# Kernel optimization log

Hardware: AMD Instinct MI355X
Metric: run time of the kernel (lower is better)

The kernel has to match this reference:

```python
import jax, jax.numpy as jnp
import numpy as np

B, T, N_EMBD = 1, 2048, 2048
N_HEAD = 16
KV_LOW = 512      # kv_low_rank == head_size (compressed value dim)
Q_LOW = 1024
ROPE_HS = 64
QK_HS = KV_LOW + ROPE_HS  # 576
HEAD_SIZE = KV_LOW        # v_equiv = c_kv.view(B,1,T,head_size)


def _rope_tables(seq_len, dim, base=10000.0):
    # litgpt-style: theta over half dim, duplicated to full dim
    inv = 1.0 / (base ** (np.arange(0, dim, 2, dtype=np.float32) / dim))
    t = np.arange(seq_len, dtype=np.float32)
    freqs = np.outer(t, inv)                      # [T, dim/2]
    emb = np.concatenate([freqs, freqs], axis=-1)  # [T, dim]
    return jnp.asarray(np.cos(emb)), jnp.asarray(np.sin(emb))


def _apply_rope(x, cos, sin):
    # x: [..., T, d]; cos/sin broadcastable [T, d]. rotate-half RoPE.
    d = x.shape[-1]
    x1, x2 = x[..., : d // 2], x[..., d // 2:]
    rotated = jnp.concatenate([-x2, x1], axis=-1)
    return x * cos + rotated * sin


def setup_inputs() -> dict:
    key = jax.random.key(0)
    ks = jax.random.split(key, 4)
    x = jax.random.normal(ks[0], (B, T, N_EMBD), dtype=jnp.float32)
    cos, sin = _rope_tables(T, ROPE_HS)
    s = 0.02
    W_qkv = jax.random.normal(ks[1], (N_EMBD, KV_LOW + ROPE_HS + Q_LOW), dtype=jnp.float32) * s
    W_qdec = jax.random.normal(ks[2], (Q_LOW, N_HEAD * QK_HS), dtype=jnp.float32) * s
    W_out = jax.random.normal(ks[3], (N_HEAD * HEAD_SIZE, N_EMBD), dtype=jnp.float32) * s
    return {"x": x, "cos": cos, "sin": sin, "W_qkv": W_qkv, "W_qdec": W_qdec, "W_out": W_out}


def reference(x, cos, sin, W_qkv, W_qdec, W_out):
    Bq, Tq, _ = x.shape
    # latent encoding and split
    latents = x @ W_qkv                                       # [B,T,kv+rope+q]
    c_kv = latents[..., :KV_LOW]                              # [B,T,512] (keys-nope and values)
    k_r = latents[..., KV_LOW:KV_LOW + ROPE_HS]               # [B,T,64]
    c_q = latents[..., KV_LOW + ROPE_HS:]                     # [B,T,1024]
    # per-head query decode
    q = (c_q @ W_qdec).reshape(Bq, Tq, N_HEAD, QK_HS)         # [B,T,H,576]
    q_nope, q_r = q[..., :KV_LOW], q[..., KV_LOW:]
    # partial RoPE
    k_r = _apply_rope(k_r, cos, sin)                          # [B,T,64]
    q_r = _apply_rope(q_r, cos[None, :, None, :], sin[None, :, None, :])  # [B,T,H,64]
    q = jnp.concatenate([q_nope, q_r], axis=-1)               # [B,T,H,576]
    q = jnp.swapaxes(q, 1, 2)                                 # [B,H,T,576]
    k = jnp.concatenate([c_kv, k_r], axis=-1)                 # [B,T,576] shared across heads
    v = c_kv                                                  # [B,T,512] shared across heads
    scale = 1.0 / jnp.sqrt(jnp.float32(HEAD_SIZE))
    scores = jnp.einsum('bhtd,bsd->bhts', q, k) * scale       # [B,H,T,T]
    causal = jnp.tril(jnp.ones((Tq, Tq), dtype=bool))
    scores = jnp.where(causal, scores, jnp.finfo(scores.dtype).min)
    attn = jax.nn.softmax(scores, axis=-1)
    y = jnp.einsum('bhts,bsd->bhtd', attn, v)                 # [B,H,T,512]
    y = jnp.swapaxes(y, 1, 2).reshape(Bq, Tq, N_HEAD * HEAD_SIZE)
    return y @ W_out                                          # [B,T,n_embd]
```

## Files before the change

### kernel.cpp

```cpp
#include <hip/hip_runtime.h>

typedef __bf16 bf16x8_t __attribute__((ext_vector_type(8)));
typedef float f32x4_t __attribute__((ext_vector_type(4)));

#define LAT_LD 1664
#define QK_DIM 576
#define V_DIM 512
#define NHEAD 16
#define TSEQ 2048
#define QLD 9216
#define YLD 8192
#define SCALE 0.044194173824159216f

__device__ __forceinline__ unsigned short f2bf(float f) {
  union { float f; unsigned int u; } v; v.f = f;
  unsigned int r = v.u + 0x7FFFu + ((v.u >> 16) & 1u);
  return (unsigned short)(r >> 16);
}

__device__ __forceinline__ void load_lds16(const unsigned short* g, unsigned short* l) {
  __builtin_amdgcn_global_load_lds((const __attribute__((address_space(1))) void*)g,
                                   (__attribute__((address_space(3))) void*)l, 16, 0, 0);
}

__global__ __launch_bounds__(256) void conv_flat(const float* __restrict__ src,
                                                 unsigned short* __restrict__ dst, int n) {
  int i = (blockIdx.x * 256 + threadIdx.x) * 4;
  if (i < n) {
    float4 v = *(const float4*)&src[i];
    ushort4 o;
    o.x = f2bf(v.x); o.y = f2bf(v.y); o.z = f2bf(v.z); o.w = f2bf(v.w);
    *(ushort4*)&dst[i] = o;
  }
}

__global__ __launch_bounds__(256) void conv_t(const float* __restrict__ src, int R, int Csrc,
                                              unsigned short* __restrict__ dst) {
  __shared__ unsigned short T[64][72];
  const int tid = threadIdx.x;
  const int r0 = blockIdx.x * 64, c0 = blockIdx.y * 64;
  const bool live = (c0 < Csrc);
#pragma unroll
  for (int it = 0; it < 4; ++it) {
    int idx = it * 256 + tid;
    int c4 = (idx >> 6) * 4;
    int r = idx & 63;
    float4 v = {0.f, 0.f, 0.f, 0.f};
    if (live) v = *(const float4*)&src[(size_t)(r0 + r) * Csrc + c0 + c4];
    T[c4 + 0][r] = f2bf(v.x);
    T[c4 + 1][r] = f2bf(v.y);
    T[c4 + 2][r] = f2bf(v.z);
    T[c4 + 3][r] = f2bf(v.w);
  }
  __syncthreads();
#pragma unroll
  for (int it = 0; it < 2; ++it) {
    int idx = it * 256 + tid;
    int cc = idx >> 3, r8 = (idx & 7) * 8;
    uint4 v = *(const uint4*)&T[cc][r8];
    *(uint4*)&dst[(size_t)(c0 + cc) * R + r0 + r8] = v;
  }
}

__global__ __launch_bounds__(256) void vtrans(const unsigned short* __restrict__ lat,
                                              unsigned short* __restrict__ vtg) {
  __shared__ unsigned short T[64][72];
  const int tid = threadIdx.x;
  const int r0 = blockIdx.x * 64, c0 = blockIdx.y * 64;
#pragma unroll
  for (int it = 0; it < 2; ++it) {
    int idx = it * 256 + tid;
    int c8 = (idx >> 6) * 8;
    int r = idx & 63;
    uint4 v = *(const uint4*)&lat[(size_t)(r0 + r) * LAT_LD + c0 + c8];
    unsigned short* pv = (unsigned short*)&v;
#pragma unroll
    for (int j = 0; j < 8; ++j) T[c8 + j][r] = pv[j];
  }
  __syncthreads();
#pragma unroll
  for (int it = 0; it < 2; ++it) {
    int idx = it * 256 + tid;
    int cc = idx >> 3, r8 = (idx & 7) * 8;
    uint4 v = *(const uint4*)&T[cc][r8];
    *(uint4*)&vtg[(size_t)(c0 + cc) * TSEQ + r0 + r8] = v;
  }
}

#define GEMM_PROLOGUE()                                                     \
  __shared__ __align__(16) unsigned short As[4096];                         \
  __shared__ __align__(16) unsigned short Bs[4096];                         \
  const int tid = threadIdx.x;                                              \
  const int wave = tid >> 6, lane = tid & 63;                               \
  const int quad = lane >> 4, l16 = lane & 15;                              \
  const int wm = wave >> 1, wn = wave & 1;                                  \
  f32x4_t acc[4][4];                                                        \
  f32x4_t zero = {0.f, 0.f, 0.f, 0.f};                                      \
  _Pragma("unroll") for (int mi = 0; mi < 4; ++mi)                          \
    _Pragma("unroll") for (int ni = 0; ni < 4; ++ni) acc[mi][ni] = zero;

#define GEMM_KLOOP(Aptr, Alda, Bptr, Bldb, M0, N0, KLEN)                    \
  for (int k0 = 0; k0 < (KLEN); k0 += 32) {                                 \
    _Pragma("unroll") for (int p2 = 0; p2 < 2; ++p2) {                      \
      int ci = p2 * 256 + tid;                                              \
      int rr2 = ci >> 2, cc2 = (ci & 3) * 8;                                \
      load_lds16(&(Aptr)[(size_t)((M0) + rr2) * (Alda) + k0 + cc2], &As[ci * 8]); \
      load_lds16(&(Bptr)[(size_t)((N0) + rr2) * (Bldb) + k0 + cc2], &Bs[ci * 8]); \
    }                                                                       \
    __syncthreads();                                                        \
    bf16x8_t af[4], bfr[4];                                                 \
    _Pragma("unroll") for (int mi = 0; mi < 4; ++mi)                        \
      af[mi] = *(const bf16x8_t*)&As[(wm * 64 + mi * 16 + l16) * 32 + quad * 8]; \
    _Pragma("unroll") for (int ni = 0; ni < 4; ++ni)                        \
      bfr[ni] = *(const bf16x8_t*)&Bs[(wn * 64 + ni * 16 + l16) * 32 + quad * 8]; \
    _Pragma("unroll") for (int mi = 0; mi < 4; ++mi)                        \
      _Pragma("unroll") for (int ni = 0; ni < 4; ++ni)                      \
        acc[mi][ni] = __builtin_amdgcn_mfma_f32_16x16x32_bf16(af[mi], bfr[ni], acc[mi][ni], 0, 0, 0); \
    __syncthreads();                                                        \
  }

template <int OUTF32>
__global__ __launch_bounds__(256, 2) void gemm_bt(
    const unsigned short* __restrict__ A, int lda,
    const unsigned short* __restrict__ Bt, int ldb,
    void* __restrict__ C, int ldc, int K) {
  const int m0 = blockIdx.y * 128, n0 = blockIdx.x * 128;
  GEMM_PROLOGUE();
  GEMM_KLOOP(A, lda, Bt, ldb, m0, n0, K);
#pragma unroll
  for (int mi = 0; mi < 4; ++mi)
#pragma unroll
    for (int ni = 0; ni < 4; ++ni)
#pragma unroll
      for (int r = 0; r < 4; ++r) {
        int row = m0 + wm * 64 + mi * 16 + quad * 4 + r;
        int col = n0 + wn * 64 + ni * 16 + l16;
        if (OUTF32)
          ((float*)C)[(size_t)row * ldc + col] = acc[mi][ni][r];
        else
          ((unsigned short*)C)[(size_t)row * ldc + col] = f2bf(acc[mi][ni][r]);
      }
}

__global__ __launch_bounds__(256, 2) void gemm_splitk(
    const unsigned short* __restrict__ A, int lda,
    const unsigned short* __restrict__ Bt, int ldb,
    float* __restrict__ P, int ldc, int Ks) {
  const int m0 = blockIdx.y * 128, n0 = blockIdx.x * 128;
  const size_t koff = (size_t)blockIdx.z * Ks;
  const unsigned short* Ap = A + koff;
  const unsigned short* Bp = Bt + koff;
  float* C = P + (size_t)blockIdx.z * ((size_t)gridDim.y * 128) * ldc;
  GEMM_PROLOGUE();
  GEMM_KLOOP(Ap, lda, Bp, ldb, m0, n0, Ks);
#pragma unroll
  for (int mi = 0; mi < 4; ++mi)
#pragma unroll
    for (int ni = 0; ni < 4; ++ni)
#pragma unroll
      for (int r = 0; r < 4; ++r) {
        int row = m0 + wm * 64 + mi * 16 + quad * 4 + r;
        int col = n0 + wn * 64 + ni * 16 + l16;
        C[(size_t)row * ldc + col] = acc[mi][ni][r];
      }
}

__global__ __launch_bounds__(256) void reduce2_bf(const float* __restrict__ p,
                                                  unsigned short* __restrict__ dst, int n) {
  int i = (blockIdx.x * 256 + threadIdx.x) * 4;
  if (i < n) {
    float4 a = *(const float4*)&p[i];
    float4 b = *(const float4*)&p[(size_t)n + i];
    ushort4 o;
    o.x = f2bf(a.x + b.x); o.y = f2bf(a.y + b.y);
    o.z = f2bf(a.z + b.z); o.w = f2bf(a.w + b.w);
    *(ushort4*)&dst[i] = o;
  }
}

__global__ __launch_bounds__(256) void reduce4_f32(const float* __restrict__ p,
                                                   float* __restrict__ dst, int n) {
  int i = (blockIdx.x * 256 + threadIdx.x) * 4;
  if (i < n) {
    float4 a = *(const float4*)&p[i];
    float4 b = *(const float4*)&p[(size_t)n + i];
    float4 c = *(const float4*)&p[2 * (size_t)n + i];
    float4 d = *(const float4*)&p[3 * (size_t)n + i];
    float4 o;
    o.x = (a.x + b.x) + (c.x + d.x);
    o.y = (a.y + b.y) + (c.y + d.y);
    o.z = (a.z + b.z) + (c.z + d.z);
    o.w = (a.w + b.w) + (c.w + d.w);
    *(float4*)&dst[i] = o;
  }
}

__global__ __launch_bounds__(256, 2) void qke_kernel(
    const unsigned short* __restrict__ qbuf,
    const unsigned short* __restrict__ lat,
    unsigned short* __restrict__ Ebuf,
    float* __restrict__ lsum, int tq0, int tq1) {
  int tx = blockIdx.x, i_l = 0, cnt = tq0 + 1;
  while (tx >= cnt) { tx -= cnt; ++i_l; ++cnt; }
  const int j = tx;
  const int ig = tq0 + i_l;
  const int h = blockIdx.y;
  const int Kp = tq1 << 7;
  const int Rp = (tq1 - tq0) << 7;
  const int r0g = ig << 7;

  const unsigned short* A = qbuf + (size_t)r0g * QLD + h * QK_DIM;
  const unsigned short* Bt = lat + (size_t)(j << 7) * LAT_LD;
  unsigned short* Eh = Ebuf + (size_t)h * Rp * Kp;

  GEMM_PROLOGUE();
  GEMM_KLOOP(A, QLD, Bt, LAT_LD, 0, 0, QK_DIM);

#pragma unroll
  for (int mi = 0; mi < 4; ++mi) {
    float rs[4] = {0.f, 0.f, 0.f, 0.f};
#pragma unroll
    for (int ni = 0; ni < 4; ++ni)
#pragma unroll
      for (int r = 0; r < 4; ++r) {
        int qr = r0g + wm * 64 + mi * 16 + quad * 4 + r;
        int key = (j << 7) + wn * 64 + ni * 16 + l16;
        float e = (key <= qr) ? __expf(acc[mi][ni][r] * SCALE) : 0.f;
        rs[r] += e;
        Eh[(size_t)(qr - (tq0 << 7)) * Kp + key] = f2bf(e);
      }
#pragma unroll
    for (int r = 0; r < 4; ++r) {
      float s = rs[r];
#pragma unroll
      for (int off = 1; off < 16; off <<= 1) s += __shfl_xor(s, off, 64);
      if (l16 == 0) {
        int qr = r0g + wm * 64 + mi * 16 + quad * 4 + r;
        atomicAdd(&lsum[h * TSEQ + qr], s);
      }
    }
  }
}

__global__ __launch_bounds__(256, 2) void pv_kernel(
    const unsigned short* __restrict__ Ebuf,
    const unsigned short* __restrict__ vtg,
    const float* __restrict__ lsum,
    unsigned short* __restrict__ ybuf, int tq0, int tq1) {
  const int i_l = blockIdx.y, h = blockIdx.z;
  const int n0 = blockIdx.x * 128;
  const int Kp = tq1 << 7;
  const int Rp = (tq1 - tq0) << 7;
  const int Kmax = (tq0 + i_l + 1) << 7;

  const unsigned short* A = Ebuf + (size_t)h * Rp * Kp + (size_t)(i_l << 7) * Kp;
  const unsigned short* Bt = vtg;

  GEMM_PROLOGUE();
  GEMM_KLOOP(A, Kp, Bt, TSEQ, 0, n0, Kmax);

#pragma unroll
  for (int mi = 0; mi < 4; ++mi)
#pragma unroll
    for (int r = 0; r < 4; ++r) {
      int row_g = ((tq0 + i_l) << 7) + wm * 64 + mi * 16 + quad * 4 + r;
      float inv = 1.f / lsum[h * TSEQ + row_g];
#pragma unroll
      for (int ni = 0; ni < 4; ++ni) {
        int col = h * V_DIM + n0 + wn * 64 + ni * 16 + l16;
        ybuf[(size_t)row_g * YLD + col] = f2bf(acc[mi][ni][r] * inv);
      }
    }
}

__global__ __launch_bounds__(256) void rope_k(unsigned short* __restrict__ lat,
                                              const float* __restrict__ cosb,
                                              const float* __restrict__ sinb) {
  int idx = blockIdx.x * 256 + threadIdx.x;
  if (idx >= TSEQ * 32) return;
  int t = idx >> 5, d = idx & 31;
  unsigned short* p = &lat[(size_t)t * LAT_LD + 512];
  union { unsigned int u; float f; } a, b;
  a.u = ((unsigned int)p[d]) << 16; b.u = ((unsigned int)p[d + 32]) << 16;
  float c0 = cosb[t * 64 + d], s0 = sinb[t * 64 + d];
  float c1 = cosb[t * 64 + d + 32], s1 = sinb[t * 64 + d + 32];
  p[d] = f2bf(a.f * c0 - b.f * s0);
  p[d + 32] = f2bf(b.f * c1 + a.f * s1);
}

__global__ __launch_bounds__(256) void rope_q(unsigned short* __restrict__ q,
                                              const float* __restrict__ cosb,
                                              const float* __restrict__ sinb) {
  int idx = blockIdx.x * 256 + threadIdx.x;
  if (idx >= TSEQ * NHEAD * 32) return;
  int t = idx >> 9, h = (idx >> 5) & 15, d = idx & 31;
  unsigned short* p = &q[(size_t)t * QLD + h * QK_DIM + 512];
  union { unsigned int u; float f; } a, b;
  a.u = ((unsigned int)p[d]) << 16; b.u = ((unsigned int)p[d + 32]) << 16;
  float c0 = cosb[t * 64 + d], s0 = sinb[t * 64 + d];
  float c1 = cosb[t * 64 + d + 32], s1 = sinb[t * 64 + d + 32];
  p[d] = f2bf(a.f * c0 - b.f * s0);
  p[d + 32] = f2bf(b.f * c1 + a.f * s1);
}

extern "C" void kernel_launch(void* const* d_in, const int* in_sizes, int n_in,
                              void* d_out, int out_size, void* d_ws, size_t ws_size,
                              hipStream_t stream) {
  (void)in_sizes; (void)n_in; (void)out_size; (void)ws_size;
  const float* x     = (const float*)d_in[0];
  const float* cosb  = (const float*)d_in[1];
  const float* sinb  = (const float*)d_in[2];
  const float* wqkv  = (const float*)d_in[3];
  const float* wqdec = (const float*)d_in[4];
  const float* wout  = (const float*)d_in[5];
  float* out = (float*)d_out;

  unsigned short* ws     = (unsigned short*)d_ws;
  unsigned short* xb     = ws;
  unsigned short* wqkvT  = xb     + (size_t)2048 * 2048;
  unsigned short* wqdecT = wqkvT  + (size_t)1664 * 2048;
  unsigned short* lat    = wqdecT + (size_t)9216 * 1024;
  unsigned short* qbuf   = lat    + (size_t)2048 * 1664;
  unsigned short* woutT  = qbuf   + (size_t)2048 * 9216;
  unsigned short* ybuf   = woutT  + (size_t)2048 * 8192;
  unsigned short* vtg    = ybuf   + (size_t)2048 * 8192;
  float*          lsumf  = (float*)(vtg + (size_t)512 * 2048);
  unsigned short* Ebuf   = ws;
  float*          P1     = (float*)qbuf;
  float*          Pf     = (float*)ws;

  conv_flat<<<4096, 256, 0, stream>>>(x, xb, 2048 * 2048);
  conv_t<<<dim3(32, 26), 256, 0, stream>>>(wqkv, 2048, 1600, wqkvT);
  conv_t<<<dim3(16, 144), 256, 0, stream>>>(wqdec, 1024, 9216, wqdecT);
  conv_t<<<dim3(128, 32), 256, 0, stream>>>(wout, 8192, 2048, woutT);
  hipMemsetAsync(lsumf, 0, NHEAD * TSEQ * sizeof(float), stream);

  gemm_splitk<<<dim3(13, 16, 2), 256, 0, stream>>>(xb, 2048, wqkvT, 2048, P1, 1664, 1024);
  reduce2_bf<<<3328, 256, 0, stream>>>(P1, lat, 2048 * 1664);
  rope_k<<<256, 256, 0, stream>>>(lat, cosb, sinb);
  vtrans<<<dim3(32, 8), 256, 0, stream>>>(lat, vtg);

  gemm_bt<0><<<dim3(72, 16), 256, 0, stream>>>(lat + 576, LAT_LD, wqdecT, 1024, qbuf, QLD, 1024);
  rope_q<<<4096, 256, 0, stream>>>(qbuf, cosb, sinb);

  qke_kernel<<<dim3(36, 16), 256, 0, stream>>>(qbuf, lat, Ebuf, lsumf, 0, 8);
  pv_kernel<<<dim3(4, 8, 16), 256, 0, stream>>>(Ebuf, vtg, lsumf, ybuf, 0, 8);
  qke_kernel<<<dim3(42, 16), 256, 0, stream>>>(qbuf, lat, Ebuf, lsumf, 8, 12);
  pv_kernel<<<dim3(4, 4, 16), 256, 0, stream>>>(Ebuf, vtg, lsumf, ybuf, 8, 12);
  qke_kernel<<<dim3(58, 16), 256, 0, stream>>>(qbuf, lat, Ebuf, lsumf, 12, 16);
  pv_kernel<<<dim3(4, 4, 16), 256, 0, stream>>>(Ebuf, vtg, lsumf, ybuf, 12, 16);

  gemm_splitk<<<dim3(16, 16, 4), 256, 0, stream>>>(ybuf, YLD, woutT, 8192, Pf, 2048, 2048);
  reduce4_f32<<<4096, 256, 0, stream>>>(Pf, out, 2048 * 2048);
}
```

Baseline: 586.5 us.

## Fuse prep kernels, fold RoPE into Q GEMM, pack attention panels

Result: faster. 544.8 us (-7.1%).

```diff
diff --git a/kernel.cpp b/kernel.cpp
--- a/kernel.cpp
+++ b/kernel.cpp
@@ -10,6 +10,7 @@
 #define TSEQ 2048
 #define QLD 9216
 #define YLD 8192
+#define KLD 576
 #define SCALE 0.044194173824159216f
 
 __device__ __forceinline__ unsigned short f2bf(float f) {
@@ -23,22 +24,11 @@
                                    (__attribute__((address_space(3))) void*)l, 16, 0, 0);
 }
 
-__global__ __launch_bounds__(256) void conv_flat(const float* __restrict__ src,
-                                                 unsigned short* __restrict__ dst, int n) {
-  int i = (blockIdx.x * 256 + threadIdx.x) * 4;
-  if (i < n) {
-    float4 v = *(const float4*)&src[i];
-    ushort4 o;
-    o.x = f2bf(v.x); o.y = f2bf(v.y); o.z = f2bf(v.z); o.w = f2bf(v.w);
-    *(ushort4*)&dst[i] = o;
-  }
-}
-
-__global__ __launch_bounds__(256) void conv_t(const float* __restrict__ src, int R, int Csrc,
-                                              unsigned short* __restrict__ dst) {
-  __shared__ unsigned short T[64][72];
-  const int tid = threadIdx.x;
-  const int r0 = blockIdx.x * 64, c0 = blockIdx.y * 64;
+__device__ __forceinline__ void conv_t_body(const float* __restrict__ src, int R, int Csrc,
+                                            unsigned short* __restrict__ dst,
+                                            int bx, int by, int tid,
+                                            unsigned short (*T)[72]) {
+  const int r0 = bx * 64, c0 = by * 64;
   const bool live = (c0 < Csrc);
 #pragma unroll
   for (int it = 0; it < 4; ++it) {
@@ -62,8 +52,38 @@
   }
 }
 
-__global__ __launch_bounds__(256) void vtrans(const unsigned short* __restrict__ lat,
-                                              unsigned short* __restrict__ vtg) {
+__global__ __launch_bounds__(256) void prep_all(
+    const float* __restrict__ x, unsigned short* __restrict__ xb,
+    const float* __restrict__ wqkv, unsigned short* __restrict__ wqkvT,
+    const float* __restrict__ wqdec, unsigned short* __restrict__ wqdecT,
+    const float* __restrict__ wout, unsigned short* __restrict__ woutT,
+    float* __restrict__ lsum) {
+  __shared__ unsigned short T[64][72];
+  const int blk = blockIdx.x, tid = threadIdx.x;
+  if (blk < 4096) {
+    int i = (blk * 256 + tid) * 4;
+    float4 v = *(const float4*)&x[i];
+    ushort4 o;
+    o.x = f2bf(v.x); o.y = f2bf(v.y); o.z = f2bf(v.z); o.w = f2bf(v.w);
+    *(ushort4*)&xb[i] = o;
+  } else if (blk < 4928) {
+    int l = blk - 4096;
+    conv_t_body(wqkv, 2048, 1600, wqkvT, l & 31, l >> 5, tid, T);
+  } else if (blk < 7232) {
+    int l = blk - 4928;
+    conv_t_body(wqdec, 1024, 9216, wqdecT, l & 15, l >> 4, tid, T);
+  } else if (blk < 11328) {
+    int l = blk - 7232;
+    conv_t_body(wout, 8192, 2048, woutT, l & 127, l >> 7, tid, T);
+  } else {
+    int i = ((blk - 11328) * 256 + tid) * 4;
+    *(float4*)&lsum[i] = (float4){0.f, 0.f, 0.f, 0.f};
+  }
+}
+
+__global__ __launch_bounds__(256) void vtrans_kcopy(const unsigned short* __restrict__ lat,
+                                                    unsigned short* __restrict__ vtg,
+                                                    unsigned short* __restrict__ kbuf) {
   __shared__ unsigned short T[64][72];
   const int tid = threadIdx.x;
   const int r0 = blockIdx.x * 64, c0 = blockIdx.y * 64;
@@ -73,6 +93,7 @@
     int c8 = (idx >> 6) * 8;
     int r = idx & 63;
     uint4 v = *(const uint4*)&lat[(size_t)(r0 + r) * LAT_LD + c0 + c8];
+    *(uint4*)&kbuf[(size_t)(r0 + r) * KLD + c0 + c8] = v;
     unsigned short* pv = (unsigned short*)&v;
 #pragma unroll
     for (int j = 0; j < 8; ++j) T[c8 + j][r] = pv[j];
@@ -85,6 +106,22 @@
     uint4 v = *(const uint4*)&T[cc][r8];
     *(uint4*)&vtg[(size_t)(c0 + cc) * TSEQ + r0 + r8] = v;
   }
+}
+
+__global__ __launch_bounds__(256) void rope_k(const unsigned short* __restrict__ lat,
+                                              unsigned short* __restrict__ kbuf,
+                                              const float* __restrict__ cosb,
+                                              const float* __restrict__ sinb) {
+  int idx = blockIdx.x * 256 + threadIdx.x;
+  if (idx >= TSEQ * 32) return;
+  int t = idx >> 5, d = idx & 31;
+  const unsigned short* p = &lat[(size_t)t * LAT_LD + 512];
+  union { unsigned int u; float f; } a, b;
+  a.u = ((unsigned int)p[d]) << 16; b.u = ((unsigned int)p[d + 32]) << 16;
+  float c0 = cosb[t * 64 + d], s0 = sinb[t * 64 + d];
+  float c1 = cosb[t * 64 + d + 32], s1 = sinb[t * 64 + d + 32];
+  kbuf[(size_t)t * KLD + 512 + d] = f2bf(a.f * c0 - b.f * s0);
+  kbuf[(size_t)t * KLD + 544 + d] = f2bf(b.f * c1 + a.f * s1);
 }
 
 #define GEMM_PROLOGUE()                                                     \
@@ -119,29 +156,6 @@
     __syncthreads();                                                        \
   }
 
-template <int OUTF32>
-__global__ __launch_bounds__(256, 2) void gemm_bt(
-    const unsigned short* __restrict__ A, int lda,
-    const unsigned short* __restrict__ Bt, int ldb,
-    void* __restrict__ C, int ldc, int K) {
-  const int m0 = blockIdx.y * 128, n0 = blockIdx.x * 128;
-  GEMM_PROLOGUE();
-  GEMM_KLOOP(A, lda, Bt, ldb, m0, n0, K);
-#pragma unroll
-  for (int mi = 0; mi < 4; ++mi)
-#pragma unroll
-    for (int ni = 0; ni < 4; ++ni)
-#pragma unroll
-      for (int r = 0; r < 4; ++r) {
-        int row = m0 + wm * 64 + mi * 16 + quad * 4 + r;
-        int col = n0 + wn * 64 + ni * 16 + l16;
-        if (OUTF32)
-          ((float*)C)[(size_t)row * ldc + col] = acc[mi][ni][r];
-        else
-          ((unsigned short*)C)[(size_t)row * ldc + col] = f2bf(acc[mi][ni][r]);
-      }
-}
-
 __global__ __launch_bounds__(256, 2) void gemm_splitk(
     const unsigned short* __restrict__ A, int lda,
     const unsigned short* __restrict__ Bt, int ldb,
@@ -163,6 +177,40 @@
         int col = n0 + wn * 64 + ni * 16 + l16;
         C[(size_t)row * ldc + col] = acc[mi][ni][r];
       }
+}
+
+__global__ __launch_bounds__(256, 2) void gemm_qdec(
+    const unsigned short* __restrict__ A,
+    const unsigned short* __restrict__ Bt,
+    unsigned short* __restrict__ qbuf,
+    const float* __restrict__ cosb, const float* __restrict__ sinb) {
+  const int m0 = blockIdx.y * 128, n0 = blockIdx.x * 128;
+  GEMM_PROLOGUE();
+  GEMM_KLOOP(A, LAT_LD, Bt, 1024, m0, n0, 1024);
+
+  const int cb = n0 + wn * 64;
+  const bool ropeh = (cb % QK_DIM) == 512;
+#pragma unroll
+  for (int mi = 0; mi < 4; ++mi)
+#pragma unroll
+    for (int r = 0; r < 4; ++r) {
+      int t = m0 + wm * 64 + mi * 16 + quad * 4 + r;
+      if (ropeh) {
+#pragma unroll
+        for (int ni = 0; ni < 2; ++ni) {
+          int d = ni * 16 + l16;
+          float c0f = cosb[t * 64 + d], s0f = sinb[t * 64 + d];
+          float c1f = cosb[t * 64 + d + 32], s1f = sinb[t * 64 + d + 32];
+          float v1 = acc[mi][ni][r], v2 = acc[mi][ni + 2][r];
+          qbuf[(size_t)t * QLD + cb + d] = f2bf(v1 * c0f - v2 * s0f);
+          qbuf[(size_t)t * QLD + cb + 32 + d] = f2bf(v2 * c1f + v1 * s1f);
+        }
+      } else {
+#pragma unroll
+        for (int ni = 0; ni < 4; ++ni)
+          qbuf[(size_t)t * QLD + cb + ni * 16 + l16] = f2bf(acc[mi][ni][r]);
+      }
+    }
 }
 
 __global__ __launch_bounds__(256) void reduce2_bf(const float* __restrict__ p,
@@ -197,24 +245,24 @@
 
 __global__ __launch_bounds__(256, 2) void qke_kernel(
     const unsigned short* __restrict__ qbuf,
-    const unsigned short* __restrict__ lat,
+    const unsigned short* __restrict__ kbuf,
     unsigned short* __restrict__ Ebuf,
     float* __restrict__ lsum, int tq0, int tq1) {
-  int tx = blockIdx.x, i_l = 0, cnt = tq0 + 1;
-  while (tx >= cnt) { tx -= cnt; ++i_l; ++cnt; }
+  int tx = blockIdx.x, ig = tq1 - 1, cnt = tq1;
+  while (tx >= cnt) { tx -= cnt; --ig; --cnt; }
   const int j = tx;
-  const int ig = tq0 + i_l;
   const int h = blockIdx.y;
-  const int Kp = tq1 << 7;
-  const int Rp = (tq1 - tq0) << 7;
+  const int Kmax = (ig + 1) << 7;
   const int r0g = ig << 7;
+  const int panelSz = (tq1 * (tq1 + 1) - tq0 * (tq0 + 1)) >> 1;
+  const int pre = (ig * (ig + 1) - tq0 * (tq0 + 1)) >> 1;
 
   const unsigned short* A = qbuf + (size_t)r0g * QLD + h * QK_DIM;
-  const unsigned short* Bt = lat + (size_t)(j << 7) * LAT_LD;
-  unsigned short* Eh = Ebuf + (size_t)h * Rp * Kp;
+  const unsigned short* Bt = kbuf + (size_t)(j << 7) * KLD;
+  unsigned short* Eh = Ebuf + ((size_t)h * panelSz + pre) * 16384;
 
   GEMM_PROLOGUE();
-  GEMM_KLOOP(A, QLD, Bt, LAT_LD, 0, 0, QK_DIM);
+  GEMM_KLOOP(A, QLD, Bt, KLD, 0, 0, QK_DIM);
 
 #pragma unroll
   for (int mi = 0; mi < 4; ++mi) {
@@ -227,7 +275,7 @@
         int key = (j << 7) + wn * 64 + ni * 16 + l16;
         float e = (key <= qr) ? __expf(acc[mi][ni][r] * SCALE) : 0.f;
         rs[r] += e;
-        Eh[(size_t)(qr - (tq0 << 7)) * Kp + key] = f2bf(e);
+        Eh[(size_t)(qr - r0g) * Kmax + key] = f2bf(e);
       }
 #pragma unroll
     for (int r = 0; r < 4; ++r) {
@@ -247,23 +295,24 @@
     const unsigned short* __restrict__ vtg,
     const float* __restrict__ lsum,
     unsigned short* __restrict__ ybuf, int tq0, int tq1) {
-  const int i_l = blockIdx.y, h = blockIdx.z;
+  const int i_l = (tq1 - tq0 - 1) - blockIdx.y;
+  const int ig = tq0 + i_l;
+  const int h = blockIdx.z;
   const int n0 = blockIdx.x * 128;
-  const int Kp = tq1 << 7;
-  const int Rp = (tq1 - tq0) << 7;
-  const int Kmax = (tq0 + i_l + 1) << 7;
-
-  const unsigned short* A = Ebuf + (size_t)h * Rp * Kp + (size_t)(i_l << 7) * Kp;
-  const unsigned short* Bt = vtg;
+  const int Kmax = (ig + 1) << 7;
+  const int panelSz = (tq1 * (tq1 + 1) - tq0 * (tq0 + 1)) >> 1;
+  const int pre = (ig * (ig + 1) - tq0 * (tq0 + 1)) >> 1;
+
+  const unsigned short* A = Ebuf + ((size_t)h * panelSz + pre) * 16384;
 
   GEMM_PROLOGUE();
-  GEMM_KLOOP(A, Kp, Bt, TSEQ, 0, n0, Kmax);
+  GEMM_KLOOP(A, Kmax, vtg, TSEQ, 0, n0, Kmax);
 
 #pragma unroll
   for (int mi = 0; mi < 4; ++mi)
 #pragma unroll
     for (int r = 0; r < 4; ++r) {
-      int row_g = ((tq0 + i_l) << 7) + wm * 64 + mi * 16 + quad * 4 + r;
+      int row_g = (ig << 7) + wm * 64 + mi * 16 + quad * 4 + r;
       float inv = 1.f / lsum[h * TSEQ + row_g];
 #pragma unroll
       for (int ni = 0; ni < 4; ++ni) {
@@ -271,36 +320,6 @@
         ybuf[(size_t)row_g * YLD + col] = f2bf(acc[mi][ni][r] * inv);
       }
     }
-}
-
-__global__ __launch_bounds__(256) void rope_k(unsigned short* __restrict__ lat,
-                                              const float* __restrict__ cosb,
-                                              const float* __restrict__ sinb) {
-  int idx = blockIdx.x * 256 + threadIdx.x;
-  if (idx >= TSEQ * 32) return;
-  int t = idx >> 5, d = idx & 31;
-  unsigned short* p = &lat[(size_t)t * LAT_LD + 512];
-  union { unsigned int u; float f; } a, b;
-  a.u = ((unsigned int)p[d]) << 16; b.u = ((unsigned int)p[d + 32]) << 16;
-  float c0 = cosb[t * 64 + d], s0 = sinb[t * 64 + d];
-  float c1 = cosb[t * 64 + d + 32], s1 = sinb[t * 64 + d + 32];
-  p[d] = f2bf(a.f * c0 - b.f * s0);
-  p[d + 32] = f2bf(b.f * c1 + a.f * s1);
-}
-
-__global__ __launch_bounds__(256) void rope_q(unsigned short* __restrict__ q,
-                                              const float* __restrict__ cosb,
-                                              const float* __restrict__ sinb) {
-  int idx = blockIdx.x * 256 + threadIdx.x;
-  if (idx >= TSEQ * NHEAD * 32) return;
-  int t = idx >> 9, h = (idx >> 5) & 15, d = idx & 31;
-  unsigned short* p = &q[(size_t)t * QLD + h * QK_DIM + 512];
-  union { unsigned int u; float f; } a, b;
-  a.u = ((unsigned int)p[d]) << 16; b.u = ((unsigned int)p[d + 32]) << 16;
-  float c0 = cosb[t * 64 + d], s0 = sinb[t * 64 + d];
-  float c1 = cosb[t * 64 + d + 32], s1 = sinb[t * 64 + d + 32];
-  p[d] = f2bf(a.f * c0 - b.f * s0);
-  p[d + 32] = f2bf(b.f * c1 + a.f * s1);
 }
 
 extern "C" void kernel_launch(void* const* d_in, const int* in_sizes, int n_in,
@@ -324,31 +343,25 @@
   unsigned short* woutT  = qbuf   + (size_t)2048 * 9216;
   unsigned short* ybuf   = woutT  + (size_t)2048 * 8192;
   unsigned short* vtg    = ybuf   + (size_t)2048 * 8192;
-  float*          lsumf  = (float*)(vtg + (size_t)512 * 2048);
+  unsigned short* kbuf   = vtg    + (size_t)512 * 2048;
+  float*          lsumf  = (float*)(kbuf + (size_t)2048 * 576);
   unsigned short* Ebuf   = ws;
   float*          P1     = (float*)qbuf;
   float*          Pf     = (float*)ws;
 
-  conv_flat<<<4096, 256, 0, stream>>>(x, xb, 2048 * 2048);
-  conv_t<<<dim3(32, 26), 256, 0, stream>>>(wqkv, 2048, 1600, wqkvT);
-  conv_t<<<dim3(16, 144), 256, 0, stream>>>(wqdec, 1024, 9216, wqdecT);
-  conv_t<<<dim3(128, 32), 256, 0, stream>>>(wout, 8192, 2048, woutT);
-  hipMemsetAsync(lsumf, 0, NHEAD * TSEQ * sizeof(float), stream);
+  prep_all<<<11360, 256, 0, stream>>>(x, xb, wqkv, wqkvT, wqdec, wqdecT, wout, woutT, lsumf);
 
   gemm_splitk<<<dim3(13, 16, 2), 256, 0, stream>>>(xb, 2048, wqkvT, 2048, P1, 1664, 1024);
   reduce2_bf<<<3328, 256, 0, stream>>>(P1, lat, 2048 * 1664);
-  rope_k<<<256, 256, 0, stream>>>(lat, cosb, sinb);
-  vtrans<<<dim3(32, 8), 256, 0, stream>>>(lat, vtg);
-
-  gemm_bt<0><<<dim3(72, 16), 256, 0, stream>>>(lat + 576, LAT_LD, wqdecT, 1024, qbuf, QLD, 1024);
-  rope_q<<<4096, 256, 0, stream>>>(qbuf, cosb, sinb);
-
-  qke_kernel<<<dim3(36, 16), 256, 0, stream>>>(qbuf, lat, Ebuf, lsumf, 0, 8);
-  pv_kernel<<<dim3(4, 8, 16), 256, 0, stream>>>(Ebuf, vtg, lsumf, ybuf, 0, 8);
-  qke_kernel<<<dim3(42, 16), 256, 0, stream>>>(qbuf, lat, Ebuf, lsumf, 8, 12);
-  pv_kernel<<<dim3(4, 4, 16), 256, 0, stream>>>(Ebuf, vtg, lsumf, ybuf, 8, 12);
-  qke_kernel<<<dim3(58, 16), 256, 0, stream>>>(qbuf, lat, Ebuf, lsumf, 12, 16);
-  pv_kernel<<<dim3(4, 4, 16), 256, 0, stream>>>(Ebuf, vtg, lsumf, ybuf, 12, 16);
+  rope_k<<<256, 256, 0, stream>>>(lat, kbuf, cosb, sinb);
+  vtrans_kcopy<<<dim3(32, 8), 256, 0, stream>>>(lat, vtg, kbuf);
+
+  gemm_qdec<<<dim3(72, 16), 256, 0, stream>>>(lat + 576, wqdecT, qbuf, cosb, sinb);
+
+  qke_kernel<<<dim3(66, 16), 256, 0, stream>>>(qbuf, kbuf, Ebuf, lsumf, 0, 11);
+  pv_kernel<<<dim3(4, 11, 16), 256, 0, stream>>>(Ebuf, vtg, lsumf, ybuf, 0, 11);
+  qke_kernel<<<dim3(70, 16), 256, 0, stream>>>(qbuf, kbuf, Ebuf, lsumf, 11, 16);
+  pv_kernel<<<dim3(4, 5, 16), 256, 0, stream>>>(Ebuf, vtg, lsumf, ybuf, 11, 16);
 
   gemm_splitk<<<dim3(16, 16, 4), 256, 0, stream>>>(ybuf, YLD, woutT, 8192, Pf, 2048, 2048);
   reduce4_f32<<<4096, 256, 0, stream>>>(Pf, out, 2048 * 2048);
```
